# Kernel optimization log

Measured on AMD Instinct MI355X. Metric: run time of the kernel, lower is better.

## Reference

```python
import jax, jax.numpy as jnp
import numpy as np

N = 2048          # num agents / graph nodes
D = 128           # n_actor == n_map
ALPHA = 0.2       # GAT leakyrelu alpha
NEG = -1e9
X_IDX = [4, 9, 14, 19]   # actors_inter_cat time indices per LSTM step
E_IDX = [0, 4, 9, 14]    # graph_adjs time indices per LSTM step


def setup_inputs() -> dict:
    key = jax.random.key(0)
    ks = jax.random.split(key, 10)
    xavier = lambda k, shape: jax.random.uniform(
        k, shape, jnp.float32, -1.0, 1.0) * 1.414 * np.sqrt(6.0 / (shape[-2] + shape[-1]))
    actors_inter_cat = jax.random.normal(ks[0], (N, 20, D), jnp.float32)
    graph_adjs = jax.random.randint(ks[1], (N, 20, N), 0, 2, jnp.int32)
    # 4 GAT_SRF gates (forget, input, input_cell, output), stacked on leading axis
    Wg = xavier(ks[2], (4, 2 * D, D))          # gate projection W: in=2*D, out=D
    ag = xavier(ks[3], (4, 2 * D))             # attention vector a (2*out_features,)
    W = xavier(ks[4], (D, D))                  # GAT cell output projection
    b = xavier(ks[5], (1, D))
    h0 = xavier(ks[6], (1, D))
    conv_w = jax.random.normal(ks[7], (3, D, D, 2), jnp.float32) * (1.0 / np.sqrt(2 * D))
    conv_b = jax.random.normal(ks[8], (3, D), jnp.float32) * 0.01
    return {"actors_inter_cat": actors_inter_cat, "graph_adjs": graph_adjs,
            "Wg": Wg, "ag": ag, "W": W, "b": b, "h0": h0,
            "conv_w": conv_w, "conv_b": conv_b}


def _gat_gates(gin, mask, Wg, ag):
    # gin: (N, 2D); mask: (N, N) bool. Computes all 4 GAT_SRF gates at once.
    Wh = jnp.einsum('nf,gfo->gno', gin, Wg)                 # (4, N, D)
    s_src = jnp.einsum('gno,go->gn', Wh, ag[:, :D])         # a^T [Wh_i ..]
    s_dst = jnp.einsum('gno,go->gn', Wh, ag[:, D:])
    e = jax.nn.leaky_relu(s_src[:, :, None] + s_dst[:, None, :], ALPHA)  # (4,N,N)
    e = jnp.where(mask[None], e, NEG)
    attn = jax.nn.softmax(e, axis=-1)
    return jax.nn.elu(jnp.einsum('gnm,gmo->gno', attn, Wh))  # concat=True -> ELU


def reference(actors_inter_cat, graph_adjs, Wg, ag, W, b, h0, conv_w, conv_b):
    n = actors_inter_cat.shape[0]
    cell = actors_inter_cat[:, 0, :]
    hidden = jnp.broadcast_to(h0, (n, D))
    outs = []
    for t in range(4):  # fixed 4-step recurrence
        X = actors_inter_cat[:, X_IDX[t], :]
        mask = graph_adjs[:, E_IDX[t], :] > 0
        gin = jnp.concatenate([X, hidden], axis=1)          # (N, 2D)
        g = _gat_gates(gin, mask, Wg, ag)                   # (4, N, D)
        forget = jax.nn.sigmoid(g[0])
        inp_gate = jax.nn.sigmoid(g[1])
        inp_cell = jnp.tanh(g[2])
        out_gate = jax.nn.sigmoid(g[3])
        cell = cell * forget + inp_gate * inp_cell
        hidden = jnp.tanh(cell) * out_gate
        outs.append(jax.nn.sigmoid(hidden @ W + b))
    y = jnp.stack(outs, axis=2)                             # (N, D, 4)
    for l in range(3):  # kernel-2 Conv1d stack: length 4 -> 3 -> 2 -> 1
        y = (jnp.einsum('nct,oc->not', y[:, :, :-1], conv_w[l, :, :, 0])
             + jnp.einsum('nct,oc->not', y[:, :, 1:], conv_w[l, :, :, 1])
             + conv_b[l][None, :, None])
    return y[:, :, 0]                                       # squeeze -> (N, D)
```

## Files before the change

kernel.cpp:

```cpp
#include <hip/hip_runtime.h>

typedef __attribute__((ext_vector_type(8))) short short8;
typedef __attribute__((ext_vector_type(4))) float floatx4;

#define MFMA16(a,b,c) __builtin_amdgcn_mfma_f32_16x16x32_bf16(a,b,c,0,0,0)

__device__ __forceinline__ unsigned short f2bf(float f){
  unsigned u = __float_as_uint(f);
  u += 0x7fffu + ((u >> 16) & 1u);
  return (unsigned short)(u >> 16);
}
__device__ __forceinline__ float sigm(float x){ return 1.f/(1.f+__expf(-x)); }


__global__ __launch_bounds__(256) void prep_kernel(const float* __restrict__ actors,
    const float* __restrict__ Wg, const float* __restrict__ cw, const int* __restrict__ adj,
    float* __restrict__ cell, unsigned short* __restrict__ WgA, float* __restrict__ cwT,
    unsigned long long* __restrict__ bm){
  int bid = blockIdx.x;
  if (bid < 1024){
    int idx = bid*256 + threadIdx.x;
    int n = idx >> 7, c = idx & 127;
    cell[idx] = actors[(size_t)n*2560 + c];
  } else if (bid < 1536){
    int e = (bid-1024)*256 + threadIdx.x;
    int g = e >> 15, o = (e >> 8) & 127, k = e & 255;
    unsigned short v = f2bf(Wg[(size_t)g*32768 + k*128 + o]);
    int off = ((o>>4)*8 + (k>>5))*512 + (((k>>3)&3)*16 + (o&15))*8 + (k&7);
    WgA[(size_t)g*32768 + off] = v;
  } else if (bid < 1728){
    int e = (bid-1536)*256 + threadIdx.x;
    int l = e >> 14, rr = e & 16383, k = rr >> 7, o = rr & 127;
    cwT[(size_t)l*32768 + k*256 + o]       = cw[(size_t)l*32768 + o*256 + k*2];
    cwT[(size_t)l*32768 + k*256 + 128 + o] = cw[(size_t)l*32768 + o*256 + k*2 + 1];
  } else {
    const int E[4] = {0,4,9,14};
    int mb = bid - 1728;
    int t = mb & 3, nblk = mb >> 2;
    int wv = threadIdx.x >> 6, lane = threadIdx.x & 63;
    int n = nblk*4 + wv;
    const int* row = adj + (size_t)n*40960 + (size_t)E[t]*2048;
    unsigned long long* outp = bm + ((size_t)t*2048 + n)*32;
    for (int it=0; it<32; ++it){
      unsigned long long bal = __ballot(row[it*64 + lane] > 0);
      if (lane == 0) outp[it] = bal;
    }
  }
}

__global__ __launch_bounds__(256) void gatewh_kernel(const float* __restrict__ actors,
    const float* __restrict__ gbuf, float* __restrict__ cell, const float* __restrict__ h0,
    const float* __restrict__ W, const float* __restrict__ bvec,
    const unsigned short* __restrict__ WgA, const float* __restrict__ ag,
    float* __restrict__ y, unsigned short* __restrict__ WhB,
    float* __restrict__ s_src, float* __restrict__ s_dst, int xoff, int t){
  __shared__ float hl[16][132];
  __shared__ __align__(16) unsigned short ginb[16*264];
  __shared__ float sredS[4][4][16], sredD[4][4][16];
  int n0 = blockIdx.x*16, tid = threadIdx.x;
  int row = tid>>4, o0 = (tid&15)*8;
  if (t == 0){
    const float* hp = h0 + o0;
    #pragma unroll
    for (int j=0;j<8;++j) hl[row][o0+j] = hp[j];
  } else {
    size_t idx = (size_t)(n0+row)*128 + o0;
    float4 ga0 = *(const float4*)(gbuf+idx),          ga1 = *(const float4*)(gbuf+idx+4);
    float4 gb0 = *(const float4*)(gbuf+262144+idx),   gb1 = *(const float4*)(gbuf+262144+idx+4);
    float4 gc0 = *(const float4*)(gbuf+524288+idx),   gc1 = *(const float4*)(gbuf+524288+idx+4);
    float4 gd0 = *(const float4*)(gbuf+786432+idx),   gd1 = *(const float4*)(gbuf+786432+idx+4);
    float4 c0 = *(const float4*)(cell+idx),           c1 = *(const float4*)(cell+idx+4);
    float fgv[8] = {ga0.x,ga0.y,ga0.z,ga0.w,ga1.x,ga1.y,ga1.z,ga1.w};
    float igv[8] = {gb0.x,gb0.y,gb0.z,gb0.w,gb1.x,gb1.y,gb1.z,gb1.w};
    float icv[8] = {gc0.x,gc0.y,gc0.z,gc0.w,gc1.x,gc1.y,gc1.z,gc1.w};
    float ogv[8] = {gd0.x,gd0.y,gd0.z,gd0.w,gd1.x,gd1.y,gd1.z,gd1.w};
    float cv[8]  = {c0.x,c0.y,c0.z,c0.w,c1.x,c1.y,c1.z,c1.w};
    float cl[8], hd[8];
    #pragma unroll
    for (int j=0;j<8;++j){
      cl[j] = cv[j]*sigm(fgv[j]) + sigm(igv[j])*tanhf(icv[j]);
      hd[j] = tanhf(cl[j])*sigm(ogv[j]);
      hl[row][o0+j] = hd[j];
    }
    *(float4*)(cell+idx)   = (float4){cl[0],cl[1],cl[2],cl[3]};
    *(float4*)(cell+idx+4) = (float4){cl[4],cl[5],cl[6],cl[7]};
  }
  __syncthreads();
  if (t >= 1){
    float acc[8];
    float4 b0 = *(const float4*)(bvec+o0), b1 = *(const float4*)(bvec+o0+4);
    acc[0]=b0.x;acc[1]=b0.y;acc[2]=b0.z;acc[3]=b0.w;acc[4]=b1.x;acc[5]=b1.y;acc[6]=b1.z;acc[7]=b1.w;
    for (int k=0;k<128;++k){
      float hv = hl[row][k];
      float4 w0 = *(const float4*)(W + (size_t)k*128 + o0);
      float4 w1 = *(const float4*)(W + (size_t)k*128 + o0 + 4);
      acc[0]+=hv*w0.x; acc[1]+=hv*w0.y; acc[2]+=hv*w0.z; acc[3]+=hv*w0.w;
      acc[4]+=hv*w1.x; acc[5]+=hv*w1.y; acc[6]+=hv*w1.z; acc[7]+=hv*w1.w;
    }
    float* yp = y + (size_t)(t-1)*262144 + (size_t)(n0+row)*128 + o0;
    #pragma unroll
    for (int j=0;j<8;++j) yp[j] = sigm(acc[j]);
  }
  {
    const float* ap = actors + (size_t)(n0+row)*2560 + xoff + o0;
    float4 a = *(const float4*)ap, bb = *(const float4*)(ap+4);
    unsigned short tmp[8] = {f2bf(a.x),f2bf(a.y),f2bf(a.z),f2bf(a.w),
                             f2bf(bb.x),f2bf(bb.y),f2bf(bb.z),f2bf(bb.w)};
    *(uint4*)&ginb[row*264 + o0] = *(const uint4*)tmp;
    unsigned short tmp2[8];
    #pragma unroll
    for (int j=0;j<8;++j) tmp2[j] = f2bf(hl[row][o0+j]);
    *(uint4*)&ginb[row*264 + 128 + o0] = *(const uint4*)tmp2;
  }
  __syncthreads();
  int w = tid>>6, lane = tid&63, quad = lane>>4, l16 = lane&15;
  int m32 = blockIdx.x>>1, min32 = (blockIdx.x&1)*16 + l16;
  int qp = min32>>3, jp = min32&7;
  for (int g=0; g<4; ++g){
    floatx4 acc0 = {0.f,0.f,0.f,0.f}, acc1 = acc0;
    const unsigned short* wa = WgA + (size_t)g*32768;
    #pragma unroll
    for (int kh=0; kh<8; ++kh){
      short8 bfr = *(const short8*)&ginb[l16*264 + kh*32 + quad*8];
      short8 a0 = *(const short8*)(wa + (size_t)(((w*2+0)*8 + kh)*64 + lane)*8);
      short8 a1 = *(const short8*)(wa + (size_t)(((w*2+1)*8 + kh)*64 + lane)*8);
      acc0 = MFMA16(a0, bfr, acc0);
      acc1 = MFMA16(a1, bfr, acc1);
    }
    float ps = 0.f, pd = 0.f;
    unsigned short* wb = WhB + (size_t)(g*8 + w*2)*32768 + m32*512 + qp*128 + jp;
    const float* agp = ag + g*256;
    #pragma unroll
    for (int i=0;i<2;++i){
      floatx4 ac = i ? acc1 : acc0;
      #pragma unroll
      for (int r=0;r<4;++r){
        int o = w*32 + i*16 + quad*4 + r;
        float v = ac[r];
        ps += v*agp[o]; pd += v*agp[128+o];
        wb[i*32768 + (quad*4+r)*8] = f2bf(v);
      }
    }
    ps += __shfl_down(ps,32); ps += __shfl_down(ps,16);
    pd += __shfl_down(pd,32); pd += __shfl_down(pd,16);
    if (lane < 16){ sredS[g][w][l16] = ps; sredD[g][w][l16] = pd; }
  }
  __syncthreads();
  if (tid < 128){
    int g = tid>>5, which = (tid>>4)&1, n = tid&15;
    float s;
    if (which) s = sredD[g][0][n]+sredD[g][1][n]+sredD[g][2][n]+sredD[g][3][n];
    else       s = sredS[g][0][n]+sredS[g][1][n]+sredS[g][2][n]+sredS[g][3][n];
    (which ? s_dst : s_src)[g*2048 + n0 + n] = s;
  }
}

__global__ __launch_bounds__(256) void attn_kernel(const unsigned char* __restrict__ bmb,
    const unsigned short* __restrict__ WhB, const float* __restrict__ s_src,
    const float* __restrict__ s_dst, float* __restrict__ gout, int t){
  __shared__ float obuf[2][16][132];
  __shared__ float zpart[4][16];
  int g = blockIdx.y, n0 = blockIdx.x*16, tid = threadIdx.x;
  int w = tid>>6, lane = tid&63, quad = lane>>4, l16 = lane&15;
  float srcv = s_src[g*2048 + n0 + l16];
  const float* sd = s_dst + g*2048;
  const unsigned char* mrow = bmb + ((size_t)t*2048 + n0 + l16)*256 + w*64;
  uint4 mq0 = *(const uint4*)mrow,      mq1 = *(const uint4*)(mrow+16);
  uint4 mq2 = *(const uint4*)(mrow+32), mq3 = *(const uint4*)(mrow+48);
  unsigned mwd[16] = {mq0.x,mq0.y,mq0.z,mq0.w, mq1.x,mq1.y,mq1.z,mq1.w,
                      mq2.x,mq2.y,mq2.z,mq2.w, mq3.x,mq3.y,mq3.z,mq3.w};
  const unsigned short* wb = WhB + (size_t)g*262144;
  float z0 = 0.f;
  floatx4 acc[8];
  #pragma unroll
  for (int j=0;j<8;++j) acc[j] = (floatx4){0.f,0.f,0.f,0.f};
  #pragma unroll
  for (int c=0; c<16; ++c){
    int mk = w*512 + c*32 + quad*8;
    float4 sa = *(const float4*)(sd + mk);
    float4 sb = *(const float4*)(sd + mk + 4);
    unsigned mb = (mwd[c] >> (quad*8)) & 0xffu;
    float sv[8] = {sa.x,sa.y,sa.z,sa.w,sb.x,sb.y,sb.z,sb.w};
    short8 a0;
    #pragma unroll
    for (int j=0;j<8;++j){
      float s = srcv + sv[j];
      s = s > 0.f ? s : 0.2f*s;
      float p = ((mb >> j) & 1u) ? __expf(s) : 0.f;
      z0 += p;
      a0[j] = (short)f2bf(p);
    }
    const unsigned short* bp = wb + (size_t)(w*16 + c)*512 + lane*8;
    #pragma unroll
    for (int o16=0; o16<8; ++o16){
      short8 bfr = *(const short8*)(bp + (size_t)o16*32768);
      acc[o16] = MFMA16(a0, bfr, acc[o16]);
    }
  }
  z0 += __shfl_down(z0,32); z0 += __shfl_down(z0,16);
  if (lane < 16) zpart[w][l16] = z0;
  if (w < 2){
    #pragma unroll
    for (int o16=0;o16<8;++o16)
      #pragma unroll
      for (int r=0;r<4;++r)
        obuf[w][quad*4+r][o16*16+l16] = acc[o16][r];
  }
  __syncthreads();
  if (w >= 2){
    #pragma unroll
    for (int o16=0;o16<8;++o16)
      #pragma unroll
      for (int r=0;r<4;++r)
        obuf[w-2][quad*4+r][o16*16+l16] += acc[o16][r];
  }
  __syncthreads();
  {
    int row = tid>>4, c0 = (tid&15)*8;
    float z = zpart[0][row]+zpart[1][row]+zpart[2][row]+zpart[3][row];
    float inv = 1.f / z;
    float* go = gout + (size_t)g*262144 + (size_t)(n0+row)*128 + c0;
    #pragma unroll
    for (int j=0;j<8;++j){
      float v = (obuf[0][row][c0+j] + obuf[1][row][c0+j]) * inv;
      go[j] = v > 0.f ? v : __expf(v) - 1.f;
    }
  }
}

__global__ __launch_bounds__(256) void convgate_kernel(const float* __restrict__ gbuf,
    const float* __restrict__ cell, const float* __restrict__ W, const float* __restrict__ bvec,
    const float* __restrict__ y, const float* __restrict__ cwT, const float* __restrict__ cb,
    float* __restrict__ out){
  __shared__ float hl[2][128];
  __shared__ float ylds[2][128][4];
  int tid = threadIdx.x;
  int r = tid >> 7, o = tid & 127;
  int n = blockIdx.x*2 + r;
  size_t idx = (size_t)n*128 + o;
  {
    float g0 = gbuf[idx], g1 = gbuf[262144+idx], g2 = gbuf[524288+idx], g3 = gbuf[786432+idx];
    float cl = cell[idx]*sigm(g0) + sigm(g1)*tanhf(g2);
    hl[r][o] = tanhf(cl)*sigm(g3);
  }
  ylds[r][o][0] = y[idx];
  ylds[r][o][1] = y[262144+idx];
  ylds[r][o][2] = y[524288+idx];
  __syncthreads();
  {
    float acc = bvec[o];
    const float* hr = hl[r];
    for (int k=0;k<128;++k) acc += hr[k]*W[(size_t)k*128+o];
    ylds[r][o][3] = sigm(acc);
  }
  __syncthreads();
  {
    const float* w = cwT;
    float a0=0.f, a1=0.f, a2=0.f;
    for (int k=0;k<128;++k){
      float w0 = w[k*256 + o], w1 = w[k*256 + 128 + o];
      float y0 = ylds[r][k][0], y1 = ylds[r][k][1], y2 = ylds[r][k][2], y3 = ylds[r][k][3];
      a0 += y0*w0 + y1*w1; a1 += y1*w0 + y2*w1; a2 += y2*w0 + y3*w1;
    }
    float bb = cb[o];
    __syncthreads();
    ylds[r][o][0] = a0+bb; ylds[r][o][1] = a1+bb; ylds[r][o][2] = a2+bb;
    __syncthreads();
  }
  {
    const float* w = cwT + 32768;
    float a0=0.f, a1=0.f;
    for (int k=0;k<128;++k){
      float w0 = w[k*256 + o], w1 = w[k*256 + 128 + o];
      float y0 = ylds[r][k][0], y1 = ylds[r][k][1], y2 = ylds[r][k][2];
      a0 += y0*w0 + y1*w1; a1 += y1*w0 + y2*w1;
    }
    float bb = cb[128 + o];
    __syncthreads();
    ylds[r][o][0] = a0+bb; ylds[r][o][1] = a1+bb;
    __syncthreads();
  }
  {
    const float* w = cwT + 65536;
    float a0=0.f;
    for (int k=0;k<128;++k){
      float w0 = w[k*256 + o], w1 = w[k*256 + 128 + o];
      a0 += ylds[r][k][0]*w0 + ylds[r][k][1]*w1;
    }
    out[idx] = a0 + cb[256 + o];
  }
}

extern "C" void kernel_launch(void* const* d_in, const int* in_sizes, int n_in,
                              void* d_out, int out_size, void* d_ws, size_t ws_size,
                              hipStream_t stream) {
  const float* actors = (const float*)d_in[0];
  const int*   adj    = (const int*)d_in[1];
  const float* Wg     = (const float*)d_in[2];
  const float* ag     = (const float*)d_in[3];
  const float* W      = (const float*)d_in[4];
  const float* b      = (const float*)d_in[5];
  const float* h0     = (const float*)d_in[6];
  const float* cw     = (const float*)d_in[7];
  const float* cb     = (const float*)d_in[8];
  float* out = (float*)d_out;

  char* ws = (char*)d_ws;
  unsigned long long* bm = (unsigned long long*)ws;
  float* cell          = (float*)(ws + (size_t)(2u<<20));
  unsigned short* WgA  = (unsigned short*)(ws + (size_t)(3u<<20));
  float* cwT           = (float*)(ws + (size_t)3407872);
  float* s_src         = (float*)(ws + (size_t)3932160);
  float* s_dst         = (float*)(ws + (size_t)3932160 + 32768);
  unsigned short* WhB  = (unsigned short*)(ws + (size_t)(4u<<20));
  float* gbuf          = (float*)(ws + (size_t)(7u<<20));
  float* yplanes       = (float*)(ws + (size_t)(11u<<20));

  const int XI[4] = {4, 9, 14, 19};

  prep_kernel<<<3776, 256, 0, stream>>>(actors, Wg, cw, adj, cell, WgA, cwT, bm);
  for (int t=0; t<4; ++t){
    gatewh_kernel<<<128, 256, 0, stream>>>(actors, gbuf, cell, h0, W, b, WgA, ag,
                                           yplanes, WhB, s_src, s_dst, XI[t]*128, t);
    attn_kernel<<<dim3(128,4), 256, 0, stream>>>((const unsigned char*)bm, WhB,
                                                 s_src, s_dst, gbuf, t);
  }
  convgate_kernel<<<1024, 256, 0, stream>>>(gbuf, cell, W, b, yplanes, cwT, cb, out);
}
```

Measured before the change: 622.2 us.

## Process 32 rows per attention block and 8 nodes per conv block with vectorized loads

The attention kernel now handles 32 destination rows per block with two MFMA accumulator sets, so each bf16 Wh fragment loaded from global memory feeds two MFMAs, halving B-operand traffic per row. The final conv/gate kernel packs 8 nodes per block with 4 outputs per thread and float4 loads, which cuts repeated weight reads per node and raises vector width. In exchange the attention grid drops to 256 blocks with higher register pressure (16 floatx4 accumulators), which lowers occupancy and may leave CUs underused.

```diff
diff --git a/kernel.cpp b/kernel.cpp
--- a/kernel.cpp
+++ b/kernel.cpp
@@ -158,70 +158,88 @@
 __global__ __launch_bounds__(256) void attn_kernel(const unsigned char* __restrict__ bmb,
     const unsigned short* __restrict__ WhB, const float* __restrict__ s_src,
     const float* __restrict__ s_dst, float* __restrict__ gout, int t){
-  __shared__ float obuf[2][16][132];
-  __shared__ float zpart[4][16];
-  int g = blockIdx.y, n0 = blockIdx.x*16, tid = threadIdx.x;
+  __shared__ float obuf[2][32][132];
+  __shared__ float zpart[4][32];
+  int g = blockIdx.y, n0 = blockIdx.x*32, tid = threadIdx.x;
   int w = tid>>6, lane = tid&63, quad = lane>>4, l16 = lane&15;
-  float srcv = s_src[g*2048 + n0 + l16];
+  float srcv0 = s_src[g*2048 + n0 + l16];
+  float srcv1 = s_src[g*2048 + n0 + 16 + l16];
   const float* sd = s_dst + g*2048;
-  const unsigned char* mrow = bmb + ((size_t)t*2048 + n0 + l16)*256 + w*64;
-  uint4 mq0 = *(const uint4*)mrow,      mq1 = *(const uint4*)(mrow+16);
-  uint4 mq2 = *(const uint4*)(mrow+32), mq3 = *(const uint4*)(mrow+48);
-  unsigned mwd[16] = {mq0.x,mq0.y,mq0.z,mq0.w, mq1.x,mq1.y,mq1.z,mq1.w,
-                      mq2.x,mq2.y,mq2.z,mq2.w, mq3.x,mq3.y,mq3.z,mq3.w};
+  const unsigned char* mr0 = bmb + ((size_t)t*2048 + n0 + l16)*256 + w*64;
+  const unsigned char* mr1 = mr0 + 16*256;
+  uint4 q0 = *(const uint4*)mr0,      q1 = *(const uint4*)(mr0+16);
+  uint4 q2 = *(const uint4*)(mr0+32), q3 = *(const uint4*)(mr0+48);
+  uint4 r0 = *(const uint4*)mr1,      r1 = *(const uint4*)(mr1+16);
+  uint4 r2 = *(const uint4*)(mr1+32), r3 = *(const uint4*)(mr1+48);
+  unsigned mwd0[16] = {q0.x,q0.y,q0.z,q0.w, q1.x,q1.y,q1.z,q1.w,
+                       q2.x,q2.y,q2.z,q2.w, q3.x,q3.y,q3.z,q3.w};
+  unsigned mwd1[16] = {r0.x,r0.y,r0.z,r0.w, r1.x,r1.y,r1.z,r1.w,
+                       r2.x,r2.y,r2.z,r2.w, r3.x,r3.y,r3.z,r3.w};
   const unsigned short* wb = WhB + (size_t)g*262144;
-  float z0 = 0.f;
-  floatx4 acc[8];
+  float z0 = 0.f, z1 = 0.f;
+  floatx4 acc0[8], acc1[8];
   #pragma unroll
-  for (int j=0;j<8;++j) acc[j] = (floatx4){0.f,0.f,0.f,0.f};
+  for (int j=0;j<8;++j){ acc0[j] = (floatx4){0.f,0.f,0.f,0.f}; acc1[j] = acc0[j]; }
   #pragma unroll
   for (int c=0; c<16; ++c){
     int mk = w*512 + c*32 + quad*8;
     float4 sa = *(const float4*)(sd + mk);
     float4 sb = *(const float4*)(sd + mk + 4);
-    unsigned mb = (mwd[c] >> (quad*8)) & 0xffu;
+    unsigned mb0 = (mwd0[c] >> (quad*8)) & 0xffu;
+    unsigned mb1 = (mwd1[c] >> (quad*8)) & 0xffu;
     float sv[8] = {sa.x,sa.y,sa.z,sa.w,sb.x,sb.y,sb.z,sb.w};
-    short8 a0;
+    short8 A0, A1;
     #pragma unroll
     for (int j=0;j<8;++j){
-      float s = srcv + sv[j];
-      s = s > 0.f ? s : 0.2f*s;
-      float p = ((mb >> j) & 1u) ? __expf(s) : 0.f;
-      z0 += p;
-      a0[j] = (short)f2bf(p);
+      float s0 = srcv0 + sv[j];
+      s0 = s0 > 0.f ? s0 : 0.2f*s0;
+      float p0 = ((mb0 >> j) & 1u) ? __expf(s0) : 0.f;
+      z0 += p0;
+      A0[j] = (short)f2bf(p0);
+      float s1 = srcv1 + sv[j];
+      s1 = s1 > 0.f ? s1 : 0.2f*s1;
+      float p1 = ((mb1 >> j) & 1u) ? __expf(s1) : 0.f;
+      z1 += p1;
+      A1[j] = (short)f2bf(p1);
     }
     const unsigned short* bp = wb + (size_t)(w*16 + c)*512 + lane*8;
     #pragma unroll
     for (int o16=0; o16<8; ++o16){
       short8 bfr = *(const short8*)(bp + (size_t)o16*32768);
-      acc[o16] = MFMA16(a0, bfr, acc[o16]);
+      acc0[o16] = MFMA16(A0, bfr, acc0[o16]);
+      acc1[o16] = MFMA16(A1, bfr, acc1[o16]);
     }
   }
   z0 += __shfl_down(z0,32); z0 += __shfl_down(z0,16);
-  if (lane < 16) zpart[w][l16] = z0;
+  z1 += __shfl_down(z1,32); z1 += __shfl_down(z1,16);
+  if (lane < 16){ zpart[w][l16] = z0; zpart[w][16+l16] = z1; }
   if (w < 2){
     #pragma unroll
     for (int o16=0;o16<8;++o16)
       #pragma unroll
-      for (int r=0;r<4;++r)
-        obuf[w][quad*4+r][o16*16+l16] = acc[o16][r];
+      for (int r=0;r<4;++r){
+        obuf[w][quad*4+r][o16*16+l16]    = acc0[o16][r];
+        obuf[w][16+quad*4+r][o16*16+l16] = acc1[o16][r];
+      }
   }
   __syncthreads();
   if (w >= 2){
     #pragma unroll
     for (int o16=0;o16<8;++o16)
       #pragma unroll
-      for (int r=0;r<4;++r)
-        obuf[w-2][quad*4+r][o16*16+l16] += acc[o16][r];
-  }
-  __syncthreads();
-  {
-    int row = tid>>4, c0 = (tid&15)*8;
+      for (int r=0;r<4;++r){
+        obuf[w-2][quad*4+r][o16*16+l16]    += acc0[o16][r];
+        obuf[w-2][16+quad*4+r][o16*16+l16] += acc1[o16][r];
+      }
+  }
+  __syncthreads();
+  {
+    int row = tid>>3, c0 = (tid&7)*16;
     float z = zpart[0][row]+zpart[1][row]+zpart[2][row]+zpart[3][row];
     float inv = 1.f / z;
     float* go = gout + (size_t)g*262144 + (size_t)(n0+row)*128 + c0;
     #pragma unroll
-    for (int j=0;j<8;++j){
+    for (int j=0;j<16;++j){
       float v = (obuf[0][row][c0+j] + obuf[1][row][c0+j]) * inv;
       go[j] = v > 0.f ? v : __expf(v) - 1.f;
     }
@@ -232,62 +250,106 @@
     const float* __restrict__ cell, const float* __restrict__ W, const float* __restrict__ bvec,
     const float* __restrict__ y, const float* __restrict__ cwT, const float* __restrict__ cb,
     float* __restrict__ out){
-  __shared__ float hl[2][128];
-  __shared__ float ylds[2][128][4];
+  __shared__ float hl[8][128];
+  __shared__ float ylds[8][128][4];
   int tid = threadIdx.x;
-  int r = tid >> 7, o = tid & 127;
-  int n = blockIdx.x*2 + r;
-  size_t idx = (size_t)n*128 + o;
-  {
-    float g0 = gbuf[idx], g1 = gbuf[262144+idx], g2 = gbuf[524288+idx], g3 = gbuf[786432+idx];
-    float cl = cell[idx]*sigm(g0) + sigm(g1)*tanhf(g2);
-    hl[r][o] = tanhf(cl)*sigm(g3);
-  }
-  ylds[r][o][0] = y[idx];
-  ylds[r][o][1] = y[262144+idx];
-  ylds[r][o][2] = y[524288+idx];
-  __syncthreads();
-  {
-    float acc = bvec[o];
+  int r = tid >> 5, o0 = (tid & 31)*4;
+  int n = blockIdx.x*8 + r;
+  size_t idx = (size_t)n*128 + o0;
+  {
+    float4 g0 = *(const float4*)(gbuf+idx),        g1 = *(const float4*)(gbuf+262144+idx);
+    float4 g2 = *(const float4*)(gbuf+524288+idx), g3 = *(const float4*)(gbuf+786432+idx);
+    float4 cv = *(const float4*)(cell+idx);
+    float fg[4]={g0.x,g0.y,g0.z,g0.w}, ig[4]={g1.x,g1.y,g1.z,g1.w};
+    float ic[4]={g2.x,g2.y,g2.z,g2.w}, og[4]={g3.x,g3.y,g3.z,g3.w};
+    float cc[4]={cv.x,cv.y,cv.z,cv.w};
+    #pragma unroll
+    for (int j=0;j<4;++j){
+      float cl = cc[j]*sigm(fg[j]) + sigm(ig[j])*tanhf(ic[j]);
+      hl[r][o0+j] = tanhf(cl)*sigm(og[j]);
+    }
+  }
+  {
+    float4 y0 = *(const float4*)(y+idx), y1 = *(const float4*)(y+262144+idx),
+           y2 = *(const float4*)(y+524288+idx);
+    float a0[4]={y0.x,y0.y,y0.z,y0.w}, a1[4]={y1.x,y1.y,y1.z,y1.w}, a2[4]={y2.x,y2.y,y2.z,y2.w};
+    #pragma unroll
+    for (int j=0;j<4;++j){
+      ylds[r][o0+j][0]=a0[j]; ylds[r][o0+j][1]=a1[j]; ylds[r][o0+j][2]=a2[j];
+    }
+  }
+  __syncthreads();
+  {
+    float4 bb = *(const float4*)(bvec+o0);
+    float acc[4] = {bb.x,bb.y,bb.z,bb.w};
     const float* hr = hl[r];
-    for (int k=0;k<128;++k) acc += hr[k]*W[(size_t)k*128+o];
-    ylds[r][o][3] = sigm(acc);
-  }
-  __syncthreads();
-  {
-    const float* w = cwT;
-    float a0=0.f, a1=0.f, a2=0.f;
-    for (int k=0;k<128;++k){
-      float w0 = w[k*256 + o], w1 = w[k*256 + 128 + o];
-      float y0 = ylds[r][k][0], y1 = ylds[r][k][1], y2 = ylds[r][k][2], y3 = ylds[r][k][3];
-      a0 += y0*w0 + y1*w1; a1 += y1*w0 + y2*w1; a2 += y2*w0 + y3*w1;
-    }
-    float bb = cb[o];
+    for (int k=0;k<128;++k){
+      float hv = hr[k];
+      float4 wv = *(const float4*)(W + (size_t)k*128 + o0);
+      acc[0]+=hv*wv.x; acc[1]+=hv*wv.y; acc[2]+=hv*wv.z; acc[3]+=hv*wv.w;
+    }
+    #pragma unroll
+    for (int j=0;j<4;++j) ylds[r][o0+j][3] = sigm(acc[j]);
+  }
+  __syncthreads();
+  {
+    float a0[4]={0,0,0,0}, a1[4]={0,0,0,0}, a2[4]={0,0,0,0};
+    for (int k=0;k<128;++k){
+      float4 w0 = *(const float4*)(cwT + k*256 + o0);
+      float4 w1 = *(const float4*)(cwT + k*256 + 128 + o0);
+      float4 yv = *(const float4*)&ylds[r][k][0];
+      float wa[4]={w0.x,w0.y,w0.z,w0.w}, wb4[4]={w1.x,w1.y,w1.z,w1.w};
+      #pragma unroll
+      for (int j=0;j<4;++j){
+        a0[j] += yv.x*wa[j] + yv.y*wb4[j];
+        a1[j] += yv.y*wa[j] + yv.z*wb4[j];
+        a2[j] += yv.z*wa[j] + yv.w*wb4[j];
+      }
+    }
+    float4 bb = *(const float4*)(cb+o0);
+    float bbv[4]={bb.x,bb.y,bb.z,bb.w};
     __syncthreads();
-    ylds[r][o][0] = a0+bb; ylds[r][o][1] = a1+bb; ylds[r][o][2] = a2+bb;
+    #pragma unroll
+    for (int j=0;j<4;++j){
+      ylds[r][o0+j][0]=a0[j]+bbv[j]; ylds[r][o0+j][1]=a1[j]+bbv[j]; ylds[r][o0+j][2]=a2[j]+bbv[j];
+    }
     __syncthreads();
   }
   {
-    const float* w = cwT + 32768;
-    float a0=0.f, a1=0.f;
-    for (int k=0;k<128;++k){
-      float w0 = w[k*256 + o], w1 = w[k*256 + 128 + o];
-      float y0 = ylds[r][k][0], y1 = ylds[r][k][1], y2 = ylds[r][k][2];
-      a0 += y0*w0 + y1*w1; a1 += y1*w0 + y2*w1;
-    }
-    float bb = cb[128 + o];
+    float a0[4]={0,0,0,0}, a1[4]={0,0,0,0};
+    for (int k=0;k<128;++k){
+      float4 w0 = *(const float4*)(cwT + 32768 + k*256 + o0);
+      float4 w1 = *(const float4*)(cwT + 32768 + k*256 + 128 + o0);
+      float4 yv = *(const float4*)&ylds[r][k][0];
+      float wa[4]={w0.x,w0.y,w0.z,w0.w}, wb4[4]={w1.x,w1.y,w1.z,w1.w};
+      #pragma unroll
+      for (int j=0;j<4;++j){
+        a0[j] += yv.x*wa[j] + yv.y*wb4[j];
+        a1[j] += yv.y*wa[j] + yv.z*wb4[j];
+      }
+    }
+    float4 bb = *(const float4*)(cb+128+o0);
+    float bbv[4]={bb.x,bb.y,bb.z,bb.w};
     __syncthreads();
-    ylds[r][o][0] = a0+bb; ylds[r][o][1] = a1+bb;
+    #pragma unroll
+    for (int j=0;j<4;++j){
+      ylds[r][o0+j][0]=a0[j]+bbv[j]; ylds[r][o0+j][1]=a1[j]+bbv[j];
+    }
     __syncthreads();
   }
   {
-    const float* w = cwT + 65536;
-    float a0=0.f;
-    for (int k=0;k<128;++k){
-      float w0 = w[k*256 + o], w1 = w[k*256 + 128 + o];
-      a0 += ylds[r][k][0]*w0 + ylds[r][k][1]*w1;
-    }
-    out[idx] = a0 + cb[256 + o];
+    float a0[4]={0,0,0,0};
+    for (int k=0;k<128;++k){
+      float4 w0 = *(const float4*)(cwT + 65536 + k*256 + o0);
+      float4 w1 = *(const float4*)(cwT + 65536 + k*256 + 128 + o0);
+      float4 yv = *(const float4*)&ylds[r][k][0];
+      float wa[4]={w0.x,w0.y,w0.z,w0.w}, wb4[4]={w1.x,w1.y,w1.z,w1.w};
+      #pragma unroll
+      for (int j=0;j<4;++j) a0[j] += yv.x*wa[j] + yv.y*wb4[j];
+    }
+    float4 bb = *(const float4*)(cb+256+o0);
+    float4 res = {a0[0]+bb.x, a0[1]+bb.y, a0[2]+bb.z, a0[3]+bb.w};
+    *(float4*)(out+idx) = res;
   }
 }
 
@@ -322,8 +384,8 @@
   for (int t=0; t<4; ++t){
     gatewh_kernel<<<128, 256, 0, stream>>>(actors, gbuf, cell, h0, W, b, WgA, ag,
                                            yplanes, WhB, s_src, s_dst, XI[t]*128, t);
-    attn_kernel<<<dim3(128,4), 256, 0, stream>>>((const unsigned char*)bm, WhB,
-                                                 s_src, s_dst, gbuf, t);
-  }
-  convgate_kernel<<<1024, 256, 0, stream>>>(gbuf, cell, W, b, yplanes, cwT, cb, out);
-}
+    attn_kernel<<<dim3(64,4), 256, 0, stream>>>((const unsigned char*)bm, WhB,
+                                                s_src, s_dst, gbuf, t);
+  }
+  convgate_kernel<<<256, 256, 0, stream>>>(gbuf, cell, W, b, yplanes, cwT, cb, out);
+}
```

Result: slower. 663.4 us (+6.6%).

## Split attention key range over eight waves; give convgate two outputs per thread

Applied to the files above, without the earlier changes.

The attention kernel now runs 512 threads per block, so each of eight waves handles 256 keys instead of four waves handling 512 each. This halves the serial MFMA chain per wave and raises the number of waves resident per CU. The cost is a larger four-way LDS reduction and more shared memory per block. The final conv/gate kernel now processes four nodes per block, with each thread computing two adjacent outputs using float2 loads, so weight loads are reused across outputs and half as many blocks are launched.

```diff
diff --git a/kernel.cpp b/kernel.cpp
--- a/kernel.cpp
+++ b/kernel.cpp
@@ -155,51 +155,49 @@
   }
 }
 
-__global__ __launch_bounds__(256) void attn_kernel(const unsigned char* __restrict__ bmb,
+__global__ __launch_bounds__(512) void attn_kernel(const unsigned char* __restrict__ bmb,
     const unsigned short* __restrict__ WhB, const float* __restrict__ s_src,
     const float* __restrict__ s_dst, float* __restrict__ gout, int t){
-  __shared__ float obuf[2][16][132];
-  __shared__ float zpart[4][16];
+  __shared__ float obuf[4][16][132];
+  __shared__ float zpart[8][16];
   int g = blockIdx.y, n0 = blockIdx.x*16, tid = threadIdx.x;
   int w = tid>>6, lane = tid&63, quad = lane>>4, l16 = lane&15;
   float srcv = s_src[g*2048 + n0 + l16];
   const float* sd = s_dst + g*2048;
-  const unsigned char* mrow = bmb + ((size_t)t*2048 + n0 + l16)*256 + w*64;
-  uint4 mq0 = *(const uint4*)mrow,      mq1 = *(const uint4*)(mrow+16);
-  uint4 mq2 = *(const uint4*)(mrow+32), mq3 = *(const uint4*)(mrow+48);
-  unsigned mwd[16] = {mq0.x,mq0.y,mq0.z,mq0.w, mq1.x,mq1.y,mq1.z,mq1.w,
-                      mq2.x,mq2.y,mq2.z,mq2.w, mq3.x,mq3.y,mq3.z,mq3.w};
+  const unsigned char* mrow = bmb + ((size_t)t*2048 + n0 + l16)*256 + w*32;
+  uint4 q0 = *(const uint4*)mrow, q1 = *(const uint4*)(mrow+16);
+  unsigned mwd[8] = {q0.x,q0.y,q0.z,q0.w, q1.x,q1.y,q1.z,q1.w};
   const unsigned short* wb = WhB + (size_t)g*262144;
   float z0 = 0.f;
   floatx4 acc[8];
   #pragma unroll
   for (int j=0;j<8;++j) acc[j] = (floatx4){0.f,0.f,0.f,0.f};
   #pragma unroll
-  for (int c=0; c<16; ++c){
-    int mk = w*512 + c*32 + quad*8;
+  for (int c=0; c<8; ++c){
+    int mk = w*256 + c*32 + quad*8;
     float4 sa = *(const float4*)(sd + mk);
     float4 sb = *(const float4*)(sd + mk + 4);
     unsigned mb = (mwd[c] >> (quad*8)) & 0xffu;
     float sv[8] = {sa.x,sa.y,sa.z,sa.w,sb.x,sb.y,sb.z,sb.w};
-    short8 a0;
+    short8 A0;
     #pragma unroll
     for (int j=0;j<8;++j){
       float s = srcv + sv[j];
       s = s > 0.f ? s : 0.2f*s;
       float p = ((mb >> j) & 1u) ? __expf(s) : 0.f;
       z0 += p;
-      a0[j] = (short)f2bf(p);
-    }
-    const unsigned short* bp = wb + (size_t)(w*16 + c)*512 + lane*8;
+      A0[j] = (short)f2bf(p);
+    }
+    const unsigned short* bp = wb + (size_t)(w*8 + c)*512 + lane*8;
     #pragma unroll
     for (int o16=0; o16<8; ++o16){
       short8 bfr = *(const short8*)(bp + (size_t)o16*32768);
-      acc[o16] = MFMA16(a0, bfr, acc[o16]);
+      acc[o16] = MFMA16(A0, bfr, acc[o16]);
     }
   }
   z0 += __shfl_down(z0,32); z0 += __shfl_down(z0,16);
   if (lane < 16) zpart[w][l16] = z0;
-  if (w < 2){
+  if (w < 4){
     #pragma unroll
     for (int o16=0;o16<8;++o16)
       #pragma unroll
@@ -207,22 +205,24 @@
         obuf[w][quad*4+r][o16*16+l16] = acc[o16][r];
   }
   __syncthreads();
-  if (w >= 2){
+  if (w >= 4){
     #pragma unroll
     for (int o16=0;o16<8;++o16)
       #pragma unroll
       for (int r=0;r<4;++r)
-        obuf[w-2][quad*4+r][o16*16+l16] += acc[o16][r];
-  }
-  __syncthreads();
-  {
-    int row = tid>>4, c0 = (tid&15)*8;
-    float z = zpart[0][row]+zpart[1][row]+zpart[2][row]+zpart[3][row];
+        obuf[w-4][quad*4+r][o16*16+l16] += acc[o16][r];
+  }
+  __syncthreads();
+  {
+    int row = tid>>5, c0 = (tid&31)*4;
+    float z = zpart[0][row]+zpart[1][row]+zpart[2][row]+zpart[3][row]
+            + zpart[4][row]+zpart[5][row]+zpart[6][row]+zpart[7][row];
     float inv = 1.f / z;
     float* go = gout + (size_t)g*262144 + (size_t)(n0+row)*128 + c0;
     #pragma unroll
-    for (int j=0;j<8;++j){
-      float v = (obuf[0][row][c0+j] + obuf[1][row][c0+j]) * inv;
+    for (int j=0;j<4;++j){
+      float v = (obuf[0][row][c0+j] + obuf[1][row][c0+j]
+               + obuf[2][row][c0+j] + obuf[3][row][c0+j]) * inv;
       go[j] = v > 0.f ? v : __expf(v) - 1.f;
     }
   }
@@ -232,62 +232,104 @@
     const float* __restrict__ cell, const float* __restrict__ W, const float* __restrict__ bvec,
     const float* __restrict__ y, const float* __restrict__ cwT, const float* __restrict__ cb,
     float* __restrict__ out){
-  __shared__ float hl[2][128];
-  __shared__ float ylds[2][128][4];
+  __shared__ float hl[4][128];
+  __shared__ float ylds[4][128][4];
   int tid = threadIdx.x;
-  int r = tid >> 7, o = tid & 127;
-  int n = blockIdx.x*2 + r;
-  size_t idx = (size_t)n*128 + o;
-  {
-    float g0 = gbuf[idx], g1 = gbuf[262144+idx], g2 = gbuf[524288+idx], g3 = gbuf[786432+idx];
-    float cl = cell[idx]*sigm(g0) + sigm(g1)*tanhf(g2);
-    hl[r][o] = tanhf(cl)*sigm(g3);
-  }
-  ylds[r][o][0] = y[idx];
-  ylds[r][o][1] = y[262144+idx];
-  ylds[r][o][2] = y[524288+idx];
-  __syncthreads();
-  {
-    float acc = bvec[o];
+  int r = tid >> 6, oc = (tid & 63)*2;
+  int n = blockIdx.x*4 + r;
+  size_t idx = (size_t)n*128 + oc;
+  {
+    float2 g0 = *(const float2*)(gbuf+idx),        g1 = *(const float2*)(gbuf+262144+idx);
+    float2 g2 = *(const float2*)(gbuf+524288+idx), g3 = *(const float2*)(gbuf+786432+idx);
+    float2 cv = *(const float2*)(cell+idx);
+    float fg[2]={g0.x,g0.y}, ig[2]={g1.x,g1.y}, ic[2]={g2.x,g2.y}, og[2]={g3.x,g3.y};
+    float cc[2]={cv.x,cv.y};
+    #pragma unroll
+    for (int j=0;j<2;++j){
+      float cl = cc[j]*sigm(fg[j]) + sigm(ig[j])*tanhf(ic[j]);
+      hl[r][oc+j] = tanhf(cl)*sigm(og[j]);
+    }
+  }
+  {
+    float2 y0 = *(const float2*)(y+idx), y1 = *(const float2*)(y+262144+idx),
+           y2 = *(const float2*)(y+524288+idx);
+    float a0[2]={y0.x,y0.y}, a1[2]={y1.x,y1.y}, a2[2]={y2.x,y2.y};
+    #pragma unroll
+    for (int j=0;j<2;++j){
+      ylds[r][oc+j][0]=a0[j]; ylds[r][oc+j][1]=a1[j]; ylds[r][oc+j][2]=a2[j];
+    }
+  }
+  __syncthreads();
+  {
+    float2 bb = *(const float2*)(bvec+oc);
+    float acc[2] = {bb.x, bb.y};
     const float* hr = hl[r];
-    for (int k=0;k<128;++k) acc += hr[k]*W[(size_t)k*128+o];
-    ylds[r][o][3] = sigm(acc);
-  }
-  __syncthreads();
-  {
-    const float* w = cwT;
-    float a0=0.f, a1=0.f, a2=0.f;
-    for (int k=0;k<128;++k){
-      float w0 = w[k*256 + o], w1 = w[k*256 + 128 + o];
-      float y0 = ylds[r][k][0], y1 = ylds[r][k][1], y2 = ylds[r][k][2], y3 = ylds[r][k][3];
-      a0 += y0*w0 + y1*w1; a1 += y1*w0 + y2*w1; a2 += y2*w0 + y3*w1;
-    }
-    float bb = cb[o];
+    for (int k=0;k<128;++k){
+      float hv = hr[k];
+      float2 wv = *(const float2*)(W + (size_t)k*128 + oc);
+      acc[0]+=hv*wv.x; acc[1]+=hv*wv.y;
+    }
+    #pragma unroll
+    for (int j=0;j<2;++j) ylds[r][oc+j][3] = sigm(acc[j]);
+  }
+  __syncthreads();
+  {
+    float a0[2]={0,0}, a1[2]={0,0}, a2[2]={0,0};
+    for (int k=0;k<128;++k){
+      float2 w0 = *(const float2*)(cwT + k*256 + oc);
+      float2 w1 = *(const float2*)(cwT + k*256 + 128 + oc);
+      float4 yv = *(const float4*)&ylds[r][k][0];
+      float wa[2]={w0.x,w0.y}, wb2[2]={w1.x,w1.y};
+      #pragma unroll
+      for (int j=0;j<2;++j){
+        a0[j] += yv.x*wa[j] + yv.y*wb2[j];
+        a1[j] += yv.y*wa[j] + yv.z*wb2[j];
+        a2[j] += yv.z*wa[j] + yv.w*wb2[j];
+      }
+    }
+    float2 bb = *(const float2*)(cb+oc);
+    float bbv[2]={bb.x,bb.y};
     __syncthreads();
-    ylds[r][o][0] = a0+bb; ylds[r][o][1] = a1+bb; ylds[r][o][2] = a2+bb;
+    #pragma unroll
+    for (int j=0;j<2;++j){
+      ylds[r][oc+j][0]=a0[j]+bbv[j]; ylds[r][oc+j][1]=a1[j]+bbv[j]; ylds[r][oc+j][2]=a2[j]+bbv[j];
+    }
     __syncthreads();
   }
   {
-    const float* w = cwT + 32768;
-    float a0=0.f, a1=0.f;
-    for (int k=0;k<128;++k){
-      float w0 = w[k*256 + o], w1 = w[k*256 + 128 + o];
-      float y0 = ylds[r][k][0], y1 = ylds[r][k][1], y2 = ylds[r][k][2];
-      a0 += y0*w0 + y1*w1; a1 += y1*w0 + y2*w1;
-    }
-    float bb = cb[128 + o];
+    float a0[2]={0,0}, a1[2]={0,0};
+    for (int k=0;k<128;++k){
+      float2 w0 = *(const float2*)(cwT + 32768 + k*256 + oc);
+      float2 w1 = *(const float2*)(cwT + 32768 + k*256 + 128 + oc);
+      float4 yv = *(const float4*)&ylds[r][k][0];
+      float wa[2]={w0.x,w0.y}, wb2[2]={w1.x,w1.y};
+      #pragma unroll
+      for (int j=0;j<2;++j){
+        a0[j] += yv.x*wa[j] + yv.y*wb2[j];
+        a1[j] += yv.y*wa[j] + yv.z*wb2[j];
+      }
+    }
+    float2 bb = *(const float2*)(cb+128+oc);
+    float bbv[2]={bb.x,bb.y};
     __syncthreads();
-    ylds[r][o][0] = a0+bb; ylds[r][o][1] = a1+bb;
+    #pragma unroll
+    for (int j=0;j<2;++j){
+      ylds[r][oc+j][0]=a0[j]+bbv[j]; ylds[r][oc+j][1]=a1[j]+bbv[j];
+    }
     __syncthreads();
   }
   {
-    const float* w = cwT + 65536;
-    float a0=0.f;
-    for (int k=0;k<128;++k){
-      float w0 = w[k*256 + o], w1 = w[k*256 + 128 + o];
-      a0 += ylds[r][k][0]*w0 + ylds[r][k][1]*w1;
-    }
-    out[idx] = a0 + cb[256 + o];
+    float a0[2]={0,0};
+    for (int k=0;k<128;++k){
+      float2 w0 = *(const float2*)(cwT + 65536 + k*256 + oc);
+      float2 w1 = *(const float2*)(cwT + 65536 + k*256 + 128 + oc);
+      float4 yv = *(const float4*)&ylds[r][k][0];
+      a0[0] += yv.x*w0.x + yv.y*w1.x;
+      a0[1] += yv.x*w0.y + yv.y*w1.y;
+    }
+    float2 bb = *(const float2*)(cb+256+oc);
+    float2 res = {a0[0]+bb.x, a0[1]+bb.y};
+    *(float2*)(out+idx) = res;
   }
 }
 
@@ -322,8 +364,8 @@
   for (int t=0; t<4; ++t){
     gatewh_kernel<<<128, 256, 0, stream>>>(actors, gbuf, cell, h0, W, b, WgA, ag,
                                            yplanes, WhB, s_src, s_dst, XI[t]*128, t);
-    attn_kernel<<<dim3(128,4), 256, 0, stream>>>((const unsigned char*)bm, WhB,
+    attn_kernel<<<dim3(128,4), 512, 0, stream>>>((const unsigned char*)bm, WhB,
                                                  s_src, s_dst, gbuf, t);
   }
-  convgate_kernel<<<1024, 256, 0, stream>>>(gbuf, cell, W, b, yplanes, cwT, cb, out);
-}
+  convgate_kernel<<<512, 256, 0, stream>>>(gbuf, cell, W, b, yplanes, cwT, cb, out);
+}
```

Result: faster. 600.1 us (-3.5%).
